# Kernel optimization log

Measured on AMD Instinct MI355X. Metric: run time of the kernel, lower is better.

## Reference

```python
import jax, jax.numpy as jnp
import numpy as np

N = 100000       # nodes
E = 3200000      # directed edges (before self-loops)
F_IN = 256       # num_node_features
HID = 8          # hidden per head (conv1)
HEADS = 8        # conv1 heads
C_OUT = 1        # conv2 out channels / heads=1


def setup_inputs() -> dict:
    key = jax.random.key(0)
    ks = jax.random.split(key, 10)
    s = 0.1
    return {
        "x": jax.random.normal(ks[0], (N, F_IN), jnp.float32),
        "edge_index": jax.random.randint(ks[1], (2, E), 0, N, dtype=jnp.int32),
        "W1": jax.random.normal(ks[2], (F_IN, HEADS * HID), jnp.float32) * s,
        "att_src1": jax.random.normal(ks[3], (HEADS, HID), jnp.float32) * s,
        "att_dst1": jax.random.normal(ks[4], (HEADS, HID), jnp.float32) * s,
        "b1": jnp.zeros((HEADS * HID,), jnp.float32),
        "W2": jax.random.normal(ks[5], (HEADS * HID, C_OUT), jnp.float32) * s,
        "att_src2": jax.random.normal(ks[6], (1, C_OUT), jnp.float32) * s,
        "att_dst2": jax.random.normal(ks[7], (1, C_OUT), jnp.float32) * s,
        "b2": jnp.zeros((C_OUT,), jnp.float32),
    }


def gat_conv(x, W, att_src, att_dst, bias, src, dst, heads, out_ch, concat):
    # PyG GATConv (eval mode): h = x @ W per head; alpha over incoming edges of dst.
    h = (x @ W).reshape(-1, heads, out_ch)                 # [N, H, C]
    a_s = jnp.einsum('nhc,hc->nh', h, att_src)             # source term
    a_d = jnp.einsum('nhc,hc->nh', h, att_dst)             # target term
    e = jax.nn.leaky_relu(a_s[src] + a_d[dst], 0.2)        # [Etot, H]
    # segment softmax over edges grouped by target node
    m = jax.ops.segment_max(e, dst, num_segments=N)
    ex = jnp.exp(e - m[dst])
    denom = jax.ops.segment_sum(ex, dst, num_segments=N)
    alpha = ex / (denom[dst] + 1e-16)                      # [Etot, H]
    out = jax.ops.segment_sum(h[src] * alpha[..., None], dst, num_segments=N)
    out = out.reshape(-1, heads * out_ch) if concat else out.mean(axis=1)
    return out + bias


def reference(x, edge_index, W1, att_src1, att_dst1, b1, W2, att_src2, att_dst2, b2):
    # add self-loops (GATConv default add_self_loops=True)
    loop = jnp.arange(N, dtype=edge_index.dtype)
    src = jnp.concatenate([edge_index[0], loop])
    dst = jnp.concatenate([edge_index[1], loop])
    # dropout layers are identity in eval mode
    h = gat_conv(x, W1, att_src1, att_dst1, b1, src, dst, HEADS, HID, True)
    h = jax.nn.elu(h)
    out = gat_conv(h, W2, att_src2, att_dst2, b2, src, dst, 1, C_OUT, False)
    return jax.nn.sigmoid(out)
```

## Files before the change

kernel.cpp:

```cpp
#include <hip/hip_runtime.h>
#include <math.h>

#define FIN 256
#define C1  64
#define NH  8
#define HID 8
#define MAXBUK 512
#define CAPLOG 14
#define SC_CHUNK 8192
#define EPT (SC_CHUNK / 512)
#define NSLICE 8
#define SLDIV 12500u

typedef unsigned short ushort_t;
typedef unsigned int uint_t;
typedef __attribute__((ext_vector_type(8))) short short8;
typedef __attribute__((ext_vector_type(4))) float f32x4;

__device__ __forceinline__ ushort_t f2bf(float f) {
    uint_t u = __float_as_uint(f);
    u += 0x7fffu + ((u >> 16) & 1u);
    return (ushort_t)(u >> 16);
}
__device__ __forceinline__ uint_t packbf2(float lo, float hi) {
    return (uint_t)f2bf(lo) | ((uint_t)f2bf(hi) << 16);
}
__device__ __forceinline__ float bf_lo(uint_t w) { return __uint_as_float(w << 16); }
__device__ __forceinline__ float bf_hi(uint_t w) { return __uint_as_float(w & 0xffff0000u); }

__device__ __forceinline__ int exscan512(int v, int* lds8, int t) {
    int lane = t & 63, w = t >> 6;
    int sc = v;
#pragma unroll
    for (int o = 1; o < 64; o <<= 1) {
        int u = __shfl_up(sc, o, 64);
        if (lane >= o) sc += u;
    }
    if (lane == 63) lds8[w] = sc;
    __syncthreads();
    int woff = 0;
#pragma unroll
    for (int i = 0; i < 8; ++i) woff += (i < w) ? lds8[i] : 0;
    return woff + sc - v;
}

__global__ void k_prep(const float* __restrict__ W, ushort_t* __restrict__ Wtg,
                       int* __restrict__ bkt_cnt) {
    int tid = blockIdx.x * 256 + threadIdx.x;
    if (tid < MAXBUK) bkt_cnt[tid] = 0;
    int c = tid >> 8;
    int k = tid & 255;
    Wtg[c * 256 + k] = f2bf(W[k * C1 + c]);
}

__device__ void dev_bscatter(const int* __restrict__ ei, int E, int N, int NBUK,
                             int* __restrict__ bkt_cnt, uint_t* __restrict__ ebuf,
                             char* smem, int bid) {
    int* hist = (int*)smem;
    int* loff = (int*)(smem + 2048);
    int* lds8 = (int*)(smem + 4096);
    uint_t* vals = (uint_t*)(smem + 4160);
    ushort_t* buks = (ushort_t*)(smem + 36928);

    const int t = threadIdx.x;
    hist[t] = 0;
    __syncthreads();

    const int Etot = E + N;
    const int base0 = bid * SC_CHUNK;
    const int lim = min(base0 + SC_CHUNK, Etot);
    const int cnt = lim - base0;

    uint_t myval[EPT];
    int myb[EPT];
#pragma unroll
    for (int i = 0; i < EPT; ++i) {
        int e = base0 + t + i * 512;
        if (e < lim) {
            int s, d;
            if (e < E) { s = ei[e]; d = ei[E + e]; } else { s = e - E; d = s; }
            myval[i] = ((uint_t)s << 8) | (uint_t)(d & 255);
            myb[i] = d >> 8;
            atomicAdd(&hist[myb[i]], 1);
        } else myb[i] = -1;
    }
    __syncthreads();

    int v = hist[t];
    int ex = exscan512(v, lds8, t);
    loff[t] = ex;
    __syncthreads();

    if (t < NBUK) {
        int c = hist[t];
        if (c) hist[t] = (t << CAPLOG) + atomicAdd(&bkt_cnt[t], c) - ex;
    }
    __syncthreads();

#pragma unroll
    for (int i = 0; i < EPT; ++i) {
        if (myb[i] >= 0) {
            int pos = atomicAdd(&loff[myb[i]], 1);
            vals[pos] = myval[i];
            buks[pos] = (ushort_t)myb[i];
        }
    }
    __syncthreads();

    for (int i = t; i < cnt; i += 512)
        ebuf[hist[buks[i]] + i] = vals[i];
}

__device__ void dev_bucket_csr(const uint_t* __restrict__ ebuf, const int* __restrict__ bkt_cnt,
                               int N, int* __restrict__ deg, int* __restrict__ off,
                               int* __restrict__ csr, char* smem, int b) {
    int* hist = (int*)smem;
    int* lds8 = (int*)(smem + 8192);
    int t = threadIdx.x;
    int beg = b << CAPLOG;
    int end = beg + bkt_cnt[b];
    for (int i = t; i < 256 * NSLICE; i += 512) hist[i] = 0;
    __syncthreads();
    for (int j = beg + t; j < end; j += 512) {
        uint_t v = ebuf[j];
        int key = ((v & 255u) << 3) | ((v >> 8) / SLDIV);
        atomicAdd(&hist[key], 1);
    }
    __syncthreads();
    if (t < 256) {
        int node = (b << 8) + t;
        if (node < N) {
            int s = 0;
#pragma unroll
            for (int i = 0; i < NSLICE; ++i) s += hist[(t << 3) | i];
            deg[node] = s;
        }
    }
    int c0 = hist[4 * t], c1 = hist[4 * t + 1], c2 = hist[4 * t + 2], c3 = hist[4 * t + 3];
    int s4 = c0 + c1 + c2 + c3;
    int base = beg + exscan512(s4, lds8, t);
    hist[4 * t]     = base;
    hist[4 * t + 1] = base + c0;
    hist[4 * t + 2] = base + c0 + c1;
    hist[4 * t + 3] = base + c0 + c1 + c2;
    __syncthreads();
    if (t < 256) {
        int node = (b << 8) + t;
        if (node < N) off[node] = hist[t << 3];
    }
    __syncthreads();
    for (int j = beg + t; j < end; j += 512) {
        uint_t v = ebuf[j];
        int key = ((v & 255u) << 3) | ((v >> 8) / SLDIV);
        int pos = atomicAdd(&hist[key], 1);
        csr[pos] = (int)(v >> 8);
    }
}

__device__ void dev_gemm1(const float* __restrict__ x, const ushort_t* __restrict__ Wtg,
                          const float* __restrict__ att_s, const float* __restrict__ att_d,
                          ushort_t* __restrict__ h1b, ushort_t* __restrict__ as1b,
                          float* __restrict__ ad1, int N, int nodeBase512) {
    const int t = threadIdx.x;
    const int wv = t >> 6, l = t & 63;
    const int l15 = l & 15, q = l >> 4;
    const int node = nodeBase512 + wv * 16 + l15;
    const bool ok = node < N;
    const float* xr = x + (size_t)(ok ? node : N - 1) * FIN;

    f32x4 acc[4];
#pragma unroll
    for (int ct = 0; ct < 4; ++ct) acc[ct] = (f32x4){0.f, 0.f, 0.f, 0.f};

    for (int kk = 0; kk < 8; ++kk) {
        const int kof = kk * 32 + q * 8;
        short8 af[4];
#pragma unroll
        for (int ct = 0; ct < 4; ++ct)
            af[ct] = *reinterpret_cast<const short8*>(&Wtg[(ct * 16 + l15) * 256 + kof]);
        const float4* xp = reinterpret_cast<const float4*>(xr + kof);
        float4 v0 = xp[0], v1 = xp[1];
        union { short8 s; uint_t u[4]; } bu;
        bu.u[0] = packbf2(v0.x, v0.y);
        bu.u[1] = packbf2(v0.z, v0.w);
        bu.u[2] = packbf2(v1.x, v1.y);
        bu.u[3] = packbf2(v1.z, v1.w);
#pragma unroll
        for (int ct = 0; ct < 4; ++ct)
            acc[ct] = __builtin_amdgcn_mfma_f32_16x16x32_bf16(af[ct], bu.s, acc[ct], 0, 0, 0);
    }

    float4 ats[4], atd4[4];
#pragma unroll
    for (int ct = 0; ct < 4; ++ct) {
        ats[ct]  = *reinterpret_cast<const float4*>(&att_s[ct * 16 + q * 4]);
        atd4[ct] = *reinterpret_cast<const float4*>(&att_d[ct * 16 + q * 4]);
    }
    const int hb = q >> 1;

    float asp[8], adp[8];
#pragma unroll
    for (int h = 0; h < 8; ++h) { asp[h] = 0.f; adp[h] = 0.f; }
#pragma unroll
    for (int ct = 0; ct < 4; ++ct) {
        f32x4 a = acc[ct];
        if (ok) {
            uint2 hv;
            hv.x = packbf2(a[0], a[1]);
            hv.y = packbf2(a[2], a[3]);
            *reinterpret_cast<uint2*>(&h1b[(size_t)node * C1 + ct * 16 + q * 4]) = hv;
        }
        int h = ct * 2 + hb;
        asp[h] = a[0] * ats[ct].x + a[1] * ats[ct].y + a[2] * ats[ct].z + a[3] * ats[ct].w;
        adp[h] = a[0] * atd4[ct].x + a[1] * atd4[ct].y + a[2] * atd4[ct].z + a[3] * atd4[ct].w;
    }
#pragma unroll
    for (int o = 16; o <= 32; o <<= 1) {
#pragma unroll
        for (int h = 0; h < 8; ++h) {
            asp[h] += __shfl_xor(asp[h], o, 64);
            adp[h] += __shfl_xor(adp[h], o, 64);
        }
    }
    if (q == 0 && ok) {
        uint4 aw;
        aw.x = packbf2(asp[0], asp[1]);
        aw.y = packbf2(asp[2], asp[3]);
        aw.z = packbf2(asp[4], asp[5]);
        aw.w = packbf2(asp[6], asp[7]);
        *reinterpret_cast<uint4*>(&as1b[(size_t)node * NH]) = aw;
        *reinterpret_cast<float4*>(&ad1[(size_t)node * NH]) =
            make_float4(adp[0], adp[1], adp[2], adp[3]);
        *reinterpret_cast<float4*>(&ad1[(size_t)node * NH + 4]) =
            make_float4(adp[4], adp[5], adp[6], adp[7]);
    }
}

__global__ __launch_bounds__(512) void k_fatA(
    const int* __restrict__ ei, int E, int N, int NBUK, int* __restrict__ bkt_cnt,
    uint_t* __restrict__ ebuf,
    const float* __restrict__ x, const ushort_t* __restrict__ Wtg,
    const float* __restrict__ ats, const float* __restrict__ atd,
    ushort_t* __restrict__ h1b, ushort_t* __restrict__ as1b, float* __restrict__ ad1,
    int nbsc)
{
    __shared__ __align__(16) char smem[53312];
    if ((int)blockIdx.x < nbsc)
        dev_bscatter(ei, E, N, NBUK, bkt_cnt, ebuf, smem, blockIdx.x);
    else
        dev_gemm1(x, Wtg, ats, atd, h1b, as1b, ad1, N, ((int)blockIdx.x - nbsc) * 128);
}

__global__ __launch_bounds__(512) void k_fatB(
    const uint_t* __restrict__ ebuf, const int* __restrict__ bkt_cnt, int N,
    int* __restrict__ deg, int* __restrict__ off, int* __restrict__ csr,
    const float* __restrict__ x, const ushort_t* __restrict__ Wtg,
    const float* __restrict__ ats, const float* __restrict__ atd,
    ushort_t* __restrict__ h1b, ushort_t* __restrict__ as1b, float* __restrict__ ad1,
    int nbuk, int nodeOfs)
{
    __shared__ __align__(16) char smem[8256];
    if ((int)blockIdx.x < nbuk)
        dev_bucket_csr(ebuf, bkt_cnt, N, deg, off, csr, smem, blockIdx.x);
    else
        dev_gemm1(x, Wtg, ats, atd, h1b, as1b, ad1, N,
                  nodeOfs + ((int)blockIdx.x - nbuk) * 128);
}

__global__ __launch_bounds__(256) void k_agg1(
    const int* __restrict__ csr, const int* __restrict__ off, const int* __restrict__ deg,
    const ushort_t* __restrict__ as1b, const float* __restrict__ ad1,
    const ushort_t* __restrict__ h1b,
    const float* __restrict__ b1, const float* __restrict__ W2,
    float* __restrict__ h2, int nBeg, int nEnd)
{
    int idx = blockIdx.x * 256 + threadIdx.x;
    int n = nBeg + (idx >> 4);
    if (n >= nEnd) return;
    int sub  = threadIdx.x & 15;
    int hp   = sub & 3;
    int slot = sub >> 2;

    int beg = off[n];
    int end = beg + deg[n];

    float adv0 = ad1[(size_t)n * NH + 2 * hp];
    float adv1 = ad1[(size_t)n * NH + 2 * hp + 1];
    float den0 = 0.f, den1 = 0.f;
    float acc[16];
#pragma unroll
    for (int k = 0; k < 16; ++k) acc[k] = 0.f;

    for (int base = beg; base < end; base += 8) {
        int ja = base + slot;
        int jb = base + 4 + slot;
        int jja = ja < end ? ja : end - 1;
        int jjb = jb < end ? jb : end - 1;
        int sa = csr[jja];
        int sb = csr[jjb];
        uint_t a2a = *reinterpret_cast<const uint_t*>(&as1b[(size_t)sa * NH + 2 * hp]);
        uint_t a2b = *reinterpret_cast<const uint_t*>(&as1b[(size_t)sb * NH + 2 * hp]);
        const uint4* hpa = reinterpret_cast<const uint4*>(&h1b[(size_t)sa * C1 + hp * 16]);
        const uint4* hpb = reinterpret_cast<const uint4*>(&h1b[(size_t)sb * C1 + hp * 16]);
        uint4 ua0 = hpa[0], ua1 = hpa[1];
        uint4 ub0 = hpb[0], ub1 = hpb[1];

        float ta0 = bf_lo(a2a) + adv0;
        float ta1 = bf_hi(a2a) + adv1;
        ta0 = fmaxf(ta0, 0.2f * ta0);
        ta1 = fmaxf(ta1, 0.2f * ta1);
        bool livea = ja < end;
        float exa0 = livea ? __expf(ta0) : 0.f;
        float exa1 = livea ? __expf(ta1) : 0.f;
        float tb0 = bf_lo(a2b) + adv0;
        float tb1 = bf_hi(a2b) + adv1;
        tb0 = fmaxf(tb0, 0.2f * tb0);
        tb1 = fmaxf(tb1, 0.2f * tb1);
        bool liveb = jb < end;
        float exb0 = liveb ? __expf(tb0) : 0.f;
        float exb1 = liveb ? __expf(tb1) : 0.f;

        den0 += exa0; den1 += exa1;
        acc[0]  = fmaf(exa0, bf_lo(ua0.x), acc[0]);
        acc[1]  = fmaf(exa0, bf_hi(ua0.x), acc[1]);
        acc[2]  = fmaf(exa0, bf_lo(ua0.y), acc[2]);
        acc[3]  = fmaf(exa0, bf_hi(ua0.y), acc[3]);
        acc[4]  = fmaf(exa0, bf_lo(ua0.z), acc[4]);
        acc[5]  = fmaf(exa0, bf_hi(ua0.z), acc[5]);
        acc[6]  = fmaf(exa0, bf_lo(ua0.w), acc[6]);
        acc[7]  = fmaf(exa0, bf_hi(ua0.w), acc[7]);
        acc[8]  = fmaf(exa1, bf_lo(ua1.x), acc[8]);
        acc[9]  = fmaf(exa1, bf_hi(ua1.x), acc[9]);
        acc[10] = fmaf(exa1, bf_lo(ua1.y), acc[10]);
        acc[11] = fmaf(exa1, bf_hi(ua1.y), acc[11]);
        acc[12] = fmaf(exa1, bf_lo(ua1.z), acc[12]);
        acc[13] = fmaf(exa1, bf_hi(ua1.z), acc[13]);
        acc[14] = fmaf(exa1, bf_lo(ua1.w), acc[14]);
        acc[15] = fmaf(exa1, bf_hi(ua1.w), acc[15]);

        den0 += exb0; den1 += exb1;
        acc[0]  = fmaf(exb0, bf_lo(ub0.x), acc[0]);
        acc[1]  = fmaf(exb0, bf_hi(ub0.x), acc[1]);
        acc[2]  = fmaf(exb0, bf_lo(ub0.y), acc[2]);
        acc[3]  = fmaf(exb0, bf_hi(ub0.y), acc[3]);
        acc[4]  = fmaf(exb0, bf_lo(ub0.z), acc[4]);
        acc[5]  = fmaf(exb0, bf_hi(ub0.z), acc[5]);
        acc[6]  = fmaf(exb0, bf_lo(ub0.w), acc[6]);
        acc[7]  = fmaf(exb0, bf_hi(ub0.w), acc[7]);
        acc[8]  = fmaf(exb1, bf_lo(ub1.x), acc[8]);
        acc[9]  = fmaf(exb1, bf_hi(ub1.x), acc[9]);
        acc[10] = fmaf(exb1, bf_lo(ub1.y), acc[10]);
        acc[11] = fmaf(exb1, bf_hi(ub1.y), acc[11]);
        acc[12] = fmaf(exb1, bf_lo(ub1.z), acc[12]);
        acc[13] = fmaf(exb1, bf_hi(ub1.z), acc[13]);
        acc[14] = fmaf(exb1, bf_lo(ub1.w), acc[14]);
        acc[15] = fmaf(exb1, bf_hi(ub1.w), acc[15]);
    }

#pragma unroll
    for (int o = 4; o <= 8; o <<= 1) {
        den0 += __shfl_xor(den0, o, 64);
        den1 += __shfl_xor(den1, o, 64);
#pragma unroll
        for (int k = 0; k < 16; ++k) acc[k] += __shfl_xor(acc[k], o, 64);
    }

    float inv0 = 1.f / (den0 + 1e-16f);
    float inv1 = 1.f / (den1 + 1e-16f);
    const float4* bp = reinterpret_cast<const float4*>(&b1[hp * 16]);
    const float4* wp = reinterpret_cast<const float4*>(&W2[hp * 16]);
    float bb[16], ww[16];
#pragma unroll
    for (int i = 0; i < 4; ++i) {
        float4 b4 = bp[i], w4 = wp[i];
        bb[4 * i] = b4.x; bb[4 * i + 1] = b4.y; bb[4 * i + 2] = b4.z; bb[4 * i + 3] = b4.w;
        ww[4 * i] = w4.x; ww[4 * i + 1] = w4.y; ww[4 * i + 2] = w4.z; ww[4 * i + 3] = w4.w;
    }
    float p = 0.f;
#pragma unroll
    for (int k = 0; k < 16; ++k) {
        float inv = (k < 8) ? inv0 : inv1;
        float v = acc[k] * inv + bb[k];
        v = v > 0.f ? v : (__expf(v) - 1.f);
        p = fmaf(v, ww[k], p);
    }
#pragma unroll
    for (int o = 1; o <= 2; o <<= 1) p += __shfl_xor(p, o, 64);
    if (sub == 0) h2[n] = p;
}

__global__ __launch_bounds__(256) void k_agg2(
    const int* __restrict__ csr, const int* __restrict__ off, const int* __restrict__ deg,
    const float* __restrict__ h2,
    const float* __restrict__ ats2, const float* __restrict__ atd2,
    const float* __restrict__ b2, float* __restrict__ out, int N)
{
    int idx = blockIdx.x * 256 + threadIdx.x;
    int n = idx >> 4;
    int l16 = threadIdx.x & 15;
    if (n >= N) return;
    int beg = off[n];
    int end = beg + deg[n];
    float a_s = ats2[0], a_d = atd2[0];
    float adv = h2[n] * a_d;
    float den = 0.f, num = 0.f;
    for (int j = beg + l16; j < end; j += 16) {
        float hs = h2[csr[j]];
        float t = fmaf(hs, a_s, adv);
        t = fmaxf(t, 0.2f * t);
        float ex = __expf(t);
        den += ex;
        num = fmaf(ex, hs, num);
    }
#pragma unroll
    for (int o = 1; o <= 8; o <<= 1) {
        den += __shfl_xor(den, o, 64);
        num += __shfl_xor(num, o, 64);
    }
    if (l16 == 0) {
        float t = num / (den + 1e-16f) + b2[0];
        out[n] = 1.f / (1.f + __expf(-t));
    }
}

extern "C" void kernel_launch(void* const* d_in, const int* in_sizes, int n_in,
                              void* d_out, int out_size, void* d_ws, size_t ws_size,
                              hipStream_t stream)
{
    const float* x    = (const float*)d_in[0];
    const int*   ei   = (const int*)d_in[1];
    const float* W1   = (const float*)d_in[2];
    const float* ats1 = (const float*)d_in[3];
    const float* atd1 = (const float*)d_in[4];
    const float* b1   = (const float*)d_in[5];
    const float* W2   = (const float*)d_in[6];
    const float* ats2 = (const float*)d_in[7];
    const float* atd2 = (const float*)d_in[8];
    const float* b2   = (const float*)d_in[9];
    float* out = (float*)d_out;

    const int N = out_size;
    const int E = in_sizes[1] / 2;
    const int Etot = E + N;
    const int NBUK = (N + 255) >> 8;
    const size_t capElems = (size_t)NBUK << CAPLOG;

    char* base = (char*)d_ws;
    uint_t* ebuf = (uint_t*)base;
    size_t ebufBytes = (capElems * sizeof(uint_t) + 255) & ~(size_t)255;
    ushort_t* h1b  = (ushort_t*)(base + ebufBytes);
    ushort_t* as1b = h1b + (size_t)N * C1;
    float* ad1 = (float*)(as1b + (size_t)N * NH);
    float* h2  = ad1 + (size_t)N * NH;
    char* pend = (char*)(h2 + N);
    size_t featEnd = ((size_t)(pend - base) + 255) & ~(size_t)255;
    int* deg     = (int*)(base + featEnd);
    int* off     = deg + N;
    int* bkt_cnt = off + N;
    int* csr     = bkt_cnt + MAXBUK;
    ushort_t* wtg = (ushort_t*)(csr + capElems);

    const int nbsc = (Etot + SC_CHUNK - 1) / SC_CHUNK;
    const int halfNodes = (((N / 2) + 127) / 128) * 128;
    const int ga = halfNodes / 128;
    const int gb = (N - halfNodes + 127) / 128;

    k_prep<<<64, 256, 0, stream>>>(W1, wtg, bkt_cnt);
    k_fatA<<<nbsc + ga, 512, 0, stream>>>(ei, E, N, NBUK, bkt_cnt, ebuf,
                                          x, wtg, ats1, atd1, h1b, as1b, ad1, nbsc);
    k_fatB<<<NBUK + gb, 512, 0, stream>>>(ebuf, bkt_cnt, N, deg, off, csr,
                                          x, wtg, ats1, atd1, h1b, as1b, ad1,
                                          NBUK, halfNodes);
    const int nh = N / 2;
    k_agg1<<<(nh * 16 + 255) / 256, 256, 0, stream>>>(csr, off, deg, as1b, ad1, h1b, b1, W2, h2, 0, nh);
    k_agg1<<<((N - nh) * 16 + 255) / 256, 256, 0, stream>>>(csr, off, deg, as1b, ad1, h1b, b1, W2, h2, nh, N);
    k_agg2<<<(N * 16 + 255) / 256, 256, 0, stream>>>(csr, off, deg, h2, ats2, atd2, b2, out, N);
}
```

Before: 336.5 us.

## Split fused scatter/GEMM kernels into separate launches and cache bucket edges in registers

```diff
diff --git a/kernel.cpp b/kernel.cpp
--- a/kernel.cpp
+++ b/kernel.cpp
@@ -11,6 +11,7 @@
 #define EPT (SC_CHUNK / 512)
 #define NSLICE 8
 #define SLDIV 12500u
+#define BCEPT 20
 
 typedef unsigned short ushort_t;
 typedef unsigned int uint_t;
@@ -53,21 +54,21 @@
     Wtg[c * 256 + k] = f2bf(W[k * C1 + c]);
 }
 
-__device__ void dev_bscatter(const int* __restrict__ ei, int E, int N, int NBUK,
-                             int* __restrict__ bkt_cnt, uint_t* __restrict__ ebuf,
-                             char* smem, int bid) {
-    int* hist = (int*)smem;
-    int* loff = (int*)(smem + 2048);
-    int* lds8 = (int*)(smem + 4096);
-    uint_t* vals = (uint_t*)(smem + 4160);
-    ushort_t* buks = (ushort_t*)(smem + 36928);
+__global__ __launch_bounds__(512) void k_bscatter(const int* __restrict__ ei, int E, int N,
+                                                  int NBUK, int* __restrict__ bkt_cnt,
+                                                  uint_t* __restrict__ ebuf) {
+    __shared__ int hist[MAXBUK];
+    __shared__ int loff[MAXBUK];
+    __shared__ int lds8[16];
+    __shared__ uint_t vals[SC_CHUNK];
+    __shared__ ushort_t buks[SC_CHUNK];
 
     const int t = threadIdx.x;
     hist[t] = 0;
     __syncthreads();
 
     const int Etot = E + N;
-    const int base0 = bid * SC_CHUNK;
+    const int base0 = blockIdx.x * SC_CHUNK;
     const int lim = min(base0 + SC_CHUNK, Etot);
     const int cnt = lim - base0;
 
@@ -111,22 +112,34 @@
         ebuf[hist[buks[i]] + i] = vals[i];
 }
 
-__device__ void dev_bucket_csr(const uint_t* __restrict__ ebuf, const int* __restrict__ bkt_cnt,
-                               int N, int* __restrict__ deg, int* __restrict__ off,
-                               int* __restrict__ csr, char* smem, int b) {
-    int* hist = (int*)smem;
-    int* lds8 = (int*)(smem + 8192);
+__global__ __launch_bounds__(512) void k_bucket_csr(const uint_t* __restrict__ ebuf,
+                                                    const int* __restrict__ bkt_cnt, int N,
+                                                    int* __restrict__ deg, int* __restrict__ off,
+                                                    int* __restrict__ csr) {
+    __shared__ int hist[256 * NSLICE];
+    __shared__ int lds8[16];
+    int b = blockIdx.x;
     int t = threadIdx.x;
     int beg = b << CAPLOG;
     int end = beg + bkt_cnt[b];
     for (int i = t; i < 256 * NSLICE; i += 512) hist[i] = 0;
     __syncthreads();
-    for (int j = beg + t; j < end; j += 512) {
-        uint_t v = ebuf[j];
-        int key = ((v & 255u) << 3) | ((v >> 8) / SLDIV);
-        atomicAdd(&hist[key], 1);
-    }
-    __syncthreads();
+
+    uint_t v[BCEPT];
+#pragma unroll
+    for (int i = 0; i < BCEPT; ++i) {
+        int j = beg + t + i * 512;
+        if (j < end) {
+            v[i] = ebuf[j];
+            atomicAdd(&hist[((v[i] & 255u) << 3) | ((v[i] >> 8) / SLDIV)], 1);
+        }
+    }
+    for (int j = beg + t + BCEPT * 512; j < end; j += 512) {
+        uint_t vv = ebuf[j];
+        atomicAdd(&hist[((vv & 255u) << 3) | ((vv >> 8) / SLDIV)], 1);
+    }
+    __syncthreads();
+
     if (t < 256) {
         int node = (b << 8) + t;
         if (node < N) {
@@ -149,22 +162,34 @@
         if (node < N) off[node] = hist[t << 3];
     }
     __syncthreads();
-    for (int j = beg + t; j < end; j += 512) {
-        uint_t v = ebuf[j];
-        int key = ((v & 255u) << 3) | ((v >> 8) / SLDIV);
+
+#pragma unroll
+    for (int i = 0; i < BCEPT; ++i) {
+        int j = beg + t + i * 512;
+        if (j < end) {
+            uint_t vv = v[i];
+            int key = ((vv & 255u) << 3) | ((vv >> 8) / SLDIV);
+            int pos = atomicAdd(&hist[key], 1);
+            csr[pos] = (int)(vv >> 8);
+        }
+    }
+    for (int j = beg + t + BCEPT * 512; j < end; j += 512) {
+        uint_t vv = ebuf[j];
+        int key = ((vv & 255u) << 3) | ((vv >> 8) / SLDIV);
         int pos = atomicAdd(&hist[key], 1);
-        csr[pos] = (int)(v >> 8);
-    }
-}
-
-__device__ void dev_gemm1(const float* __restrict__ x, const ushort_t* __restrict__ Wtg,
-                          const float* __restrict__ att_s, const float* __restrict__ att_d,
-                          ushort_t* __restrict__ h1b, ushort_t* __restrict__ as1b,
-                          float* __restrict__ ad1, int N, int nodeBase512) {
+        csr[pos] = (int)(vv >> 8);
+    }
+}
+
+__global__ __launch_bounds__(256) void k_gemm1(
+    const float* __restrict__ x, const ushort_t* __restrict__ Wtg,
+    const float* __restrict__ att_s, const float* __restrict__ att_d,
+    ushort_t* __restrict__ h1b, ushort_t* __restrict__ as1b, float* __restrict__ ad1, int N)
+{
     const int t = threadIdx.x;
     const int wv = t >> 6, l = t & 63;
     const int l15 = l & 15, q = l >> 4;
-    const int node = nodeBase512 + wv * 16 + l15;
+    const int node = blockIdx.x * 64 + wv * 16 + l15;
     const bool ok = node < N;
     const float* xr = x + (size_t)(ok ? node : N - 1) * FIN;
 
@@ -234,37 +259,6 @@
         *reinterpret_cast<float4*>(&ad1[(size_t)node * NH + 4]) =
             make_float4(adp[4], adp[5], adp[6], adp[7]);
     }
-}
-
-__global__ __launch_bounds__(512) void k_fatA(
-    const int* __restrict__ ei, int E, int N, int NBUK, int* __restrict__ bkt_cnt,
-    uint_t* __restrict__ ebuf,
-    const float* __restrict__ x, const ushort_t* __restrict__ Wtg,
-    const float* __restrict__ ats, const float* __restrict__ atd,
-    ushort_t* __restrict__ h1b, ushort_t* __restrict__ as1b, float* __restrict__ ad1,
-    int nbsc)
-{
-    __shared__ __align__(16) char smem[53312];
-    if ((int)blockIdx.x < nbsc)
-        dev_bscatter(ei, E, N, NBUK, bkt_cnt, ebuf, smem, blockIdx.x);
-    else
-        dev_gemm1(x, Wtg, ats, atd, h1b, as1b, ad1, N, ((int)blockIdx.x - nbsc) * 128);
-}
-
-__global__ __launch_bounds__(512) void k_fatB(
-    const uint_t* __restrict__ ebuf, const int* __restrict__ bkt_cnt, int N,
-    int* __restrict__ deg, int* __restrict__ off, int* __restrict__ csr,
-    const float* __restrict__ x, const ushort_t* __restrict__ Wtg,
-    const float* __restrict__ ats, const float* __restrict__ atd,
-    ushort_t* __restrict__ h1b, ushort_t* __restrict__ as1b, float* __restrict__ ad1,
-    int nbuk, int nodeOfs)
-{
-    __shared__ __align__(16) char smem[8256];
-    if ((int)blockIdx.x < nbuk)
-        dev_bucket_csr(ebuf, bkt_cnt, N, deg, off, csr, smem, blockIdx.x);
-    else
-        dev_gemm1(x, Wtg, ats, atd, h1b, as1b, ad1, N,
-                  nodeOfs + ((int)blockIdx.x - nbuk) * 128);
 }
 
 __global__ __launch_bounds__(256) void k_agg1(
@@ -461,16 +455,11 @@
     ushort_t* wtg = (ushort_t*)(csr + capElems);
 
     const int nbsc = (Etot + SC_CHUNK - 1) / SC_CHUNK;
-    const int halfNodes = (((N / 2) + 127) / 128) * 128;
-    const int ga = halfNodes / 128;
-    const int gb = (N - halfNodes + 127) / 128;
 
     k_prep<<<64, 256, 0, stream>>>(W1, wtg, bkt_cnt);
-    k_fatA<<<nbsc + ga, 512, 0, stream>>>(ei, E, N, NBUK, bkt_cnt, ebuf,
-                                          x, wtg, ats1, atd1, h1b, as1b, ad1, nbsc);
-    k_fatB<<<NBUK + gb, 512, 0, stream>>>(ebuf, bkt_cnt, N, deg, off, csr,
-                                          x, wtg, ats1, atd1, h1b, as1b, ad1,
-                                          NBUK, halfNodes);
+    k_bscatter<<<nbsc, 512, 0, stream>>>(ei, E, N, NBUK, bkt_cnt, ebuf);
+    k_bucket_csr<<<NBUK, 512, 0, stream>>>(ebuf, bkt_cnt, N, deg, off, csr);
+    k_gemm1<<<(N + 63) / 64, 256, 0, stream>>>(x, wtg, ats1, atd1, h1b, as1b, ad1, N);
     const int nh = N / 2;
     k_agg1<<<(nh * 16 + 255) / 256, 256, 0, stream>>>(csr, off, deg, as1b, ad1, h1b, b1, W2, h2, 0, nh);
     k_agg1<<<((N - nh) * 16 + 255) / 256, 256, 0, stream>>>(csr, off, deg, as1b, ad1, h1b, b1, W2, h2, nh, N);
```

After: 330.3 us. Within noise of the previous version (-1.8%).
